# Kernel optimization log

Measured on AMD Instinct MI355X. Metric: run time of the kernel, lower is better.

Reference implementation:

```python
import jax, jax.numpy as jnp
import numpy as np

B, T, ND, SD, H = 4096, 256, 16, 8, 64
IN = SD + ND  # LSTM input dim


def setup_inputs() -> dict:
    key = jax.random.key(0)
    ks = jax.random.split(key, 20)
    def w(k, shape):
        fan_in = shape[0]
        return jax.random.normal(k, shape, jnp.float32) / np.sqrt(fan_in)
    return {
        "noise": jax.random.normal(ks[0], (B, T - 1, ND), jnp.float32),
        "eps": jax.random.normal(ks[1], (B, T - 1, SD), jnp.float32),
        "Wx": w(ks[2], (IN, 4 * H)),
        "Wh": w(ks[3], (H, 4 * H)),
        "b": jnp.zeros((4 * H,), jnp.float32),
        "Wm1": w(ks[4], (H, H)), "bm1": jnp.zeros((H,), jnp.float32),
        "Wm2": w(ks[5], (H, H)), "bm2": jnp.zeros((H,), jnp.float32),
        "Wm3": w(ks[6], (H, SD)), "bm3": jnp.zeros((SD,), jnp.float32),
        "Wv1": w(ks[7], (H, H)), "bv1": jnp.zeros((H,), jnp.float32),
        "Wv2": w(ks[8], (H, H)), "bv2": jnp.zeros((H,), jnp.float32),
        "Wv3": w(ks[9], (H, SD)), "bv3": jnp.zeros((SD,), jnp.float32),
    }


def reference(noise, eps, Wx, Wh, b, Wm1, bm1, Wm2, bm2, Wm3, bm3,
              Wv1, bv1, Wv2, bv2, Wv3, bv3):
    Bn = noise.shape[0]
    Hn = Wh.shape[0]
    Dn = Wm3.shape[1]

    def mlp(h, W1, b1, W2, b2, W3, b3):
        a = jax.nn.relu(h @ W1 + b1)
        a = jax.nn.relu(a @ W2 + b2)
        return a @ W3 + b3

    def step(carry, inp_t):
        x, h, c = carry
        n_t, e_t = inp_t
        # Keras LSTM: gates ordered i, f, g(cell), o
        z = jnp.concatenate([x, n_t], axis=-1) @ Wx + h @ Wh + b  # [B, 4H]
        i, f, g, o = jnp.split(z, 4, axis=-1)
        c = jax.nn.sigmoid(f) * c + jax.nn.sigmoid(i) * jnp.tanh(g)
        h = jax.nn.sigmoid(o) * jnp.tanh(c)
        mu = mlp(h, Wm1, bm1, Wm2, bm2, Wm3, bm3)
        std = jnp.exp(0.5 * mlp(h, Wv1, bv1, Wv2, bv2, Wv3, bv3))
        x = mu + std * e_t  # reparameterized Normal(mu, std).sample()
        return (x, h, c), x

    x0 = jnp.zeros((Bn, Dn), noise.dtype)  # log_series=True -> zeros
    h0 = jnp.zeros((Bn, Hn), noise.dtype)
    c0 = jnp.zeros((Bn, Hn), noise.dtype)
    noise_t = jnp.swapaxes(noise, 0, 1)  # [T-1, B, ND]
    eps_t = jnp.swapaxes(eps, 0, 1)      # [T-1, B, SD]
    _, xs = jax.lax.scan(step, (x0, h0, c0), (noise_t, eps_t))
    seq = jnp.concatenate([x0[:, None, :], jnp.swapaxes(xs, 0, 1)], axis=1)  # [B, T, SD]
    return jnp.cumsum(seq, axis=1)
```

## Files before the change

kernel.cpp:

```cpp
#include <hip/hip_runtime.h>

typedef _Float16 half8 __attribute__((ext_vector_type(8)));
typedef _Float16 half4 __attribute__((ext_vector_type(4)));
typedef float f32x4 __attribute__((ext_vector_type(4)));

#define TSTEPS 255
#define R 16
#define BLK 512
#define XSH 104
#define ASH 72

__device__ __forceinline__ float frcp(float x) { return __builtin_amdgcn_rcpf(x); }

__device__ __forceinline__ f32x4 mfma16(half8 a, half8 b, f32x4 c) {
  return __builtin_amdgcn_mfma_f32_16x16x32_f16(a, b, c, 0, 0, 0);
}

__global__ __launch_bounds__(BLK)
void genlstm_kernel(const float* __restrict__ noise,
                    const float* __restrict__ eps,
                    const float* __restrict__ Wx,
                    const float* __restrict__ Wh,
                    const float* __restrict__ bg,
                    const float* __restrict__ Wm1, const float* __restrict__ bm1,
                    const float* __restrict__ Wm2, const float* __restrict__ bm2,
                    const float* __restrict__ Wm3, const float* __restrict__ bm3,
                    const float* __restrict__ Wv1, const float* __restrict__ bv1,
                    const float* __restrict__ Wv2, const float* __restrict__ bv2,
                    const float* __restrict__ Wv3, const float* __restrict__ bv3,
                    float* __restrict__ out)
{
  __shared__ __align__(16) _Float16 xh[2][R][XSH];
  __shared__ __align__(16) _Float16 xl[2][R][XSH];
  __shared__ __align__(16) _Float16 a1h[2][R][ASH];
  __shared__ __align__(16) _Float16 a1l[2][R][ASH];
  __shared__ __align__(16) _Float16 a2h[2][R][ASH];
  __shared__ __align__(16) _Float16 a2l[2][R][ASH];

  const int tid  = threadIdx.x;
  const int w    = tid >> 6;
  const int l    = tid & 63;
  const int lrow = l & 15;
  const int lq   = l >> 4;
  const long rowbase = (long)blockIdx.x * R;

  half8 gAhi[2][3], gAlo[2][3];
  #pragma unroll
  for (int t = 0; t < 2; ++t) {
    const int T = 2 * w + t;
    const int n = 64 * (lrow & 3) + 4 * T + (lrow >> 2);
    #pragma unroll
    for (int kt = 0; kt < 3; ++kt)
      #pragma unroll
      for (int j = 0; j < 8; ++j) {
        int k = 32 * kt + 8 * lq + j;
        float v = 0.f;
        if (k < 64) v = Wh[k * 256 + n];
        else if (k < 88) v = Wx[(k - 64) * 256 + n];
        _Float16 h = (_Float16)v;
        gAhi[t][kt][j] = h;
        gAlo[t][kt][j] = (_Float16)(v - (float)h);
      }
  }

  const int chain = w >> 2;
  const int nt = w & 3;
  const float* W1 = chain ? Wv1 : Wm1;
  const float* W2 = chain ? Wv2 : Wm2;
  half8 B1hi[2], B1lo[2], B2hi[2], B2lo[2];
  #pragma unroll
  for (int kt = 0; kt < 2; ++kt)
    #pragma unroll
    for (int j = 0; j < 8; ++j) {
      int k = 32 * kt + 8 * lq + j;
      int n = 16 * nt + lrow;
      float v1 = W1[k * 64 + n];
      _Float16 h1 = (_Float16)v1;
      B1hi[kt][j] = h1; B1lo[kt][j] = (_Float16)(v1 - (float)h1);
      float v2 = W2[k * 64 + n];
      _Float16 h2 = (_Float16)v2;
      B2hi[kt][j] = h2; B2lo[kt][j] = (_Float16)(v2 - (float)h2);
    }

  half8 Amhi[2], Amlo[2], Avhi[2], Avlo[2];
  #pragma unroll
  for (int kt = 0; kt < 2; ++kt)
    #pragma unroll
    for (int j = 0; j < 8; ++j) {
      int k = 32 * kt + 8 * lq + j;
      float vm = (lrow < 8) ? Wm3[k * 8 + lrow] : 0.f;
      _Float16 hm = (_Float16)vm;
      Amhi[kt][j] = hm; Amlo[kt][j] = (_Float16)(vm - (float)hm);
      float vv = (lrow < 8) ? Wv3[k * 8 + lrow] : 0.f;
      _Float16 hv = (_Float16)vv;
      Avhi[kt][j] = hv; Avlo[kt][j] = (_Float16)(vv - (float)hv);
    }

  const float bias1 = (chain ? bv1 : bm1)[16 * nt + lrow];
  const float bias2 = (chain ? bv2 : bm2)[16 * nt + lrow];

  const int hc1 = 8 * w + lq, hc2 = hc1 + 4;
  const float4 bgA = {bg[hc1], bg[64 + hc1], bg[128 + hc1], bg[192 + hc1]};
  const float4 bgB = {bg[hc2], bg[64 + hc2], bg[128 + hc2], bg[192 + hc2]};

  const int d0 = 4 * (lq & 1);
  const float4 bm3q = *(const float4*)&bm3[d0];
  const float4 bv3q = *(const float4*)&bv3[d0];

  float cst0 = 0.f, cst1 = 0.f;
  f32x4 cum4 = {0.f, 0.f, 0.f, 0.f};
  float4 ep4 = {0.f, 0.f, 0.f, 0.f};

  half8 hHi[2], hLo[2];
  #pragma unroll
  for (int kt = 0; kt < 2; ++kt)
    #pragma unroll
    for (int j = 0; j < 8; ++j) { hHi[kt][j] = (_Float16)0; hLo[kt][j] = (_Float16)0; }

  for (int i = tid; i < 2 * R * XSH; i += BLK) {
    (&xh[0][0][0])[i] = (_Float16)0;
    (&xl[0][0][0])[i] = (_Float16)0;
  }
  {
    const int r5 = tid >> 3, d5 = tid & 7;
    if (tid < 128) out[((rowbase + r5) * 256) * 8 + d5] = 0.f;
  }

  float4 nz = {0.f, 0.f, 0.f, 0.f};
  if (tid < 64) {
    int r = tid >> 2, j4 = (tid & 3) * 4;
    float4 n0 = *(const float4*)&noise[((rowbase + r) * TSTEPS) * 16 + j4];
    float tmp[4] = {n0.x, n0.y, n0.z, n0.w};
    half4 nh, nl;
    #pragma unroll
    for (int j = 0; j < 4; ++j) {
      _Float16 h = (_Float16)tmp[j];
      nh[j] = h; nl[j] = (_Float16)(tmp[j] - (float)h);
    }
    *(half4*)&xh[0][r][72 + j4] = nh;
    *(half4*)&xl[0][r][72 + j4] = nl;
    nz = *(const float4*)&noise[((rowbase + r) * TSTEPS + 1) * 16 + j4];
  }
  if (w == 0 && lq < 2)
    ep4 = *(const float4*)&eps[((rowbase + lrow) * TSTEPS) * 8 + d0];
  __syncthreads();

  for (int ts = 0; ts < TSTEPS; ++ts) {
    const int p = ts & 1, p1 = p ^ 1;

    half8 Xhi = *(const half8*)&xh[p][lrow][64 + 8 * lq];
    half8 Xlo = *(const half8*)&xl[p][lrow][64 + 8 * lq];

    f32x4 az0 = {0.f, 0.f, 0.f, 0.f};
    f32x4 az1 = {0.f, 0.f, 0.f, 0.f};
    az0 = mfma16(gAhi[0][0], hHi[0], az0);
    az1 = mfma16(gAhi[1][0], hHi[0], az1);
    az0 = mfma16(gAlo[0][0], hHi[0], az0);
    az1 = mfma16(gAlo[1][0], hHi[0], az1);
    az0 = mfma16(gAhi[0][0], hLo[0], az0);
    az1 = mfma16(gAhi[1][0], hLo[0], az1);
    az0 = mfma16(gAhi[0][1], hHi[1], az0);
    az1 = mfma16(gAhi[1][1], hHi[1], az1);
    az0 = mfma16(gAlo[0][1], hHi[1], az0);
    az1 = mfma16(gAlo[1][1], hHi[1], az1);
    az0 = mfma16(gAhi[0][1], hLo[1], az0);
    az1 = mfma16(gAhi[1][1], hLo[1], az1);
    az0 = mfma16(gAhi[0][2], Xhi, az0);
    az1 = mfma16(gAhi[1][2], Xhi, az1);
    az0 = mfma16(gAlo[0][2], Xhi, az0);
    az1 = mfma16(gAlo[1][2], Xhi, az1);
    az0 = mfma16(gAhi[0][2], Xlo, az0);
    az1 = mfma16(gAhi[1][2], Xlo, az1);

    {
      float zi = az0[0] + bgA.x, zf = az0[1] + bgA.y;
      float zg = az0[2] + bgA.z, zo = az0[3] + bgA.w;
      float si = frcp(1.f + __expf(-zi));
      float sf = frcp(1.f + __expf(-zf));
      float so = frcp(1.f + __expf(-zo));
      float ag = fabsf(zg), eg = __expf(-2.f * ag);
      float tg = copysignf((1.f - eg) * frcp(1.f + eg), zg);
      cst0 = fmaf(sf, cst0, si * tg);
      float ac = fabsf(cst0), ec = __expf(-2.f * ac);
      float tc = copysignf((1.f - ec) * frcp(1.f + ec), cst0);
      float hv = so * tc;
      _Float16 hh = (_Float16)hv;
      xh[p1][lrow][hc1] = hh;
      xl[p1][lrow][hc1] = (_Float16)(hv - (float)hh);
    }
    {
      float zi = az1[0] + bgB.x, zf = az1[1] + bgB.y;
      float zg = az1[2] + bgB.z, zo = az1[3] + bgB.w;
      float si = frcp(1.f + __expf(-zi));
      float sf = frcp(1.f + __expf(-zf));
      float so = frcp(1.f + __expf(-zo));
      float ag = fabsf(zg), eg = __expf(-2.f * ag);
      float tg = copysignf((1.f - eg) * frcp(1.f + eg), zg);
      cst1 = fmaf(sf, cst1, si * tg);
      float ac = fabsf(cst1), ec = __expf(-2.f * ac);
      float tc = copysignf((1.f - ec) * frcp(1.f + ec), cst1);
      float hv = so * tc;
      _Float16 hh = (_Float16)hv;
      xh[p1][lrow][hc2] = hh;
      xl[p1][lrow][hc2] = (_Float16)(hv - (float)hh);
    }
    if (tid < 64) {
      int r = tid >> 2, j4 = (tid & 3) * 4;
      float tmp[4] = {nz.x, nz.y, nz.z, nz.w};
      half4 nh, nl;
      #pragma unroll
      for (int j = 0; j < 4; ++j) {
        _Float16 h = (_Float16)tmp[j];
        nh[j] = h; nl[j] = (_Float16)(tmp[j] - (float)h);
      }
      *(half4*)&xh[p1][r][72 + j4] = nh;
      *(half4*)&xl[p1][r][72 + j4] = nl;
      if (ts + 2 < TSTEPS)
        nz = *(const float4*)&noise[((rowbase + r) * TSTEPS + ts + 2) * 16 + j4];
    }
    __syncthreads();

    {
      hHi[0] = *(const half8*)&xh[p1][lrow][8 * lq];
      hHi[1] = *(const half8*)&xh[p1][lrow][32 + 8 * lq];
      hLo[0] = *(const half8*)&xl[p1][lrow][8 * lq];
      hLo[1] = *(const half8*)&xl[p1][lrow][32 + 8 * lq];
      f32x4 acc = {0.f, 0.f, 0.f, 0.f};
      #pragma unroll
      for (int kt = 0; kt < 2; ++kt) {
        acc = mfma16(hHi[kt], B1hi[kt], acc);
        acc = mfma16(hLo[kt], B1hi[kt], acc);
        acc = mfma16(hHi[kt], B1lo[kt], acc);
      }
      const int r0 = 4 * lq;
      #pragma unroll
      for (int k = 0; k < 4; ++k) {
        float v = fmaxf(acc[k] + bias1, 0.f);
        _Float16 vh = (_Float16)v;
        a1h[chain][r0 + k][16 * nt + lrow] = vh;
        a1l[chain][r0 + k][16 * nt + lrow] = (_Float16)(v - (float)vh);
      }
    }
    __syncthreads();

    {
      half8 ahi0 = *(const half8*)&a1h[chain][lrow][8 * lq];
      half8 ahi1 = *(const half8*)&a1h[chain][lrow][32 + 8 * lq];
      half8 alo0 = *(const half8*)&a1l[chain][lrow][8 * lq];
      half8 alo1 = *(const half8*)&a1l[chain][lrow][32 + 8 * lq];
      f32x4 acc = {0.f, 0.f, 0.f, 0.f};
      acc = mfma16(ahi0, B2hi[0], acc);
      acc = mfma16(alo0, B2hi[0], acc);
      acc = mfma16(ahi0, B2lo[0], acc);
      acc = mfma16(ahi1, B2hi[1], acc);
      acc = mfma16(alo1, B2hi[1], acc);
      acc = mfma16(ahi1, B2lo[1], acc);
      const int r0 = 4 * lq;
      #pragma unroll
      for (int k = 0; k < 4; ++k) {
        float v = fmaxf(acc[k] + bias2, 0.f);
        _Float16 vh = (_Float16)v;
        a2h[chain][r0 + k][16 * nt + lrow] = vh;
        a2l[chain][r0 + k][16 * nt + lrow] = (_Float16)(v - (float)vh);
      }
    }
    __syncthreads();

    if (w == 0) {
      half8 b0h0 = *(const half8*)&a2h[0][lrow][8 * lq];
      half8 b0h1 = *(const half8*)&a2h[0][lrow][32 + 8 * lq];
      half8 b0l0 = *(const half8*)&a2l[0][lrow][8 * lq];
      half8 b0l1 = *(const half8*)&a2l[0][lrow][32 + 8 * lq];
      f32x4 accm = {0.f, 0.f, 0.f, 0.f};
      accm = mfma16(Amhi[0], b0h0, accm);
      accm = mfma16(Amlo[0], b0h0, accm);
      accm = mfma16(Amhi[0], b0l0, accm);
      accm = mfma16(Amhi[1], b0h1, accm);
      accm = mfma16(Amlo[1], b0h1, accm);
      accm = mfma16(Amhi[1], b0l1, accm);
      half8 b1h0 = *(const half8*)&a2h[1][lrow][8 * lq];
      half8 b1h1 = *(const half8*)&a2h[1][lrow][32 + 8 * lq];
      half8 b1l0 = *(const half8*)&a2l[1][lrow][8 * lq];
      half8 b1l1 = *(const half8*)&a2l[1][lrow][32 + 8 * lq];
      f32x4 accv = {0.f, 0.f, 0.f, 0.f};
      accv = mfma16(Avhi[0], b1h0, accv);
      accv = mfma16(Avlo[0], b1h0, accv);
      accv = mfma16(Avhi[0], b1l0, accv);
      accv = mfma16(Avhi[1], b1h1, accv);
      accv = mfma16(Avlo[1], b1h1, accv);
      accv = mfma16(Avhi[1], b1l1, accv);

      float xs0 = fmaf(__expf(0.5f * (accv[0] + bv3q.x)), ep4.x, accm[0] + bm3q.x);
      float xs1 = fmaf(__expf(0.5f * (accv[1] + bv3q.y)), ep4.y, accm[1] + bm3q.y);
      float xs2 = fmaf(__expf(0.5f * (accv[2] + bv3q.z)), ep4.z, accm[2] + bm3q.z);
      float xs3 = fmaf(__expf(0.5f * (accv[3] + bv3q.w)), ep4.w, accm[3] + bm3q.w);
      cum4[0] += xs0; cum4[1] += xs1; cum4[2] += xs2; cum4[3] += xs3;
      if (lq < 2) {
        float4 cv = {cum4[0], cum4[1], cum4[2], cum4[3]};
        *(float4*)&out[((rowbase + lrow) * 256 + ts + 1) * 8 + d0] = cv;
        float xs[4] = {xs0, xs1, xs2, xs3};
        half4 xhv, xlv;
        #pragma unroll
        for (int j = 0; j < 4; ++j) {
          _Float16 hh = (_Float16)xs[j];
          xhv[j] = hh; xlv[j] = (_Float16)(xs[j] - (float)hh);
        }
        *(half4*)&xh[p1][lrow][64 + d0] = xhv;
        *(half4*)&xl[p1][lrow][64 + d0] = xlv;
        if (ts + 1 < TSTEPS)
          ep4 = *(const float4*)&eps[((rowbase + lrow) * TSTEPS + ts + 1) * 8 + d0];
      }
    }
    __syncthreads();
  }
}

extern "C" void kernel_launch(void* const* d_in, const int* in_sizes, int n_in,
                              void* d_out, int out_size, void* d_ws, size_t ws_size,
                              hipStream_t stream) {
  const float* noise = (const float*)d_in[0];
  const float* eps   = (const float*)d_in[1];
  const float* Wx    = (const float*)d_in[2];
  const float* Wh    = (const float*)d_in[3];
  const float* bg    = (const float*)d_in[4];
  const float* Wm1   = (const float*)d_in[5];
  const float* bm1   = (const float*)d_in[6];
  const float* Wm2   = (const float*)d_in[7];
  const float* bm2   = (const float*)d_in[8];
  const float* Wm3   = (const float*)d_in[9];
  const float* bm3   = (const float*)d_in[10];
  const float* Wv1   = (const float*)d_in[11];
  const float* bv1   = (const float*)d_in[12];
  const float* Wv2   = (const float*)d_in[13];
  const float* bv2   = (const float*)d_in[14];
  const float* Wv3   = (const float*)d_in[15];
  const float* bv3   = (const float*)d_in[16];
  float* out = (float*)d_out;

  dim3 grid(4096 / R), block(BLK);
  hipLaunchKernelGGL(genlstm_kernel, grid, block, 0, stream,
                     noise, eps, Wx, Wh, bg, Wm1, bm1, Wm2, bm2, Wm3, bm3,
                     Wv1, bv1, Wv2, bv2, Wv3, bv3, out);
}
```

Before: 544.7 us.

## Hoist recurrent h@Wh MFMAs off critical path and use LDS-only barriers

The recurrent gate contribution h@Wh is now computed right after the MLP stages, while wave 0 runs the output head, so the next step only adds the x-part MFMAs before the gate nonlinearity. __syncthreads is replaced by an lgkmcnt-only wait plus s_barrier, which no longer waits on outstanding global loads or stores. The noise staging moves from wave 0 to wave 6 to unload the wave that does the output head, and the output store is moved after the LDS writes. The risk is that the LDS-only barrier relies on global memory not being used for synchronisation between threads.

```diff
diff --git a/kernel.cpp b/kernel.cpp
--- a/kernel.cpp
+++ b/kernel.cpp
@@ -14,6 +14,25 @@
 
 __device__ __forceinline__ f32x4 mfma16(half8 a, half8 b, f32x4 c) {
   return __builtin_amdgcn_mfma_f32_16x16x32_f16(a, b, c, 0, 0, 0);
+}
+
+__device__ __forceinline__ void barrier_lds() {
+  asm volatile("s_waitcnt lgkmcnt(0)" ::: "memory");
+  __builtin_amdgcn_s_barrier();
+}
+
+__device__ __forceinline__ float gate_nl(const f32x4& az, const float4& bq, float& cs) {
+  float zi = az[0] + bq.x, zf = az[1] + bq.y;
+  float zg = az[2] + bq.z, zo = az[3] + bq.w;
+  float si = frcp(1.f + __expf(-zi));
+  float sf = frcp(1.f + __expf(-zf));
+  float so = frcp(1.f + __expf(-zo));
+  float ag = fabsf(zg), eg = __expf(-2.f * ag);
+  float tg = copysignf((1.f - eg) * frcp(1.f + eg), zg);
+  cs = fmaf(sf, cs, si * tg);
+  float ac = fabsf(cs), ec = __expf(-2.f * ac);
+  float tc = copysignf((1.f - ec) * frcp(1.f + ec), cs);
+  return so * tc;
 }
 
 __global__ __launch_bounds__(BLK)
@@ -110,6 +129,7 @@
   float cst0 = 0.f, cst1 = 0.f;
   f32x4 cum4 = {0.f, 0.f, 0.f, 0.f};
   float4 ep4 = {0.f, 0.f, 0.f, 0.f};
+  const f32x4 fzero = {0.f, 0.f, 0.f, 0.f};
 
   half8 hHi[2], hLo[2];
   #pragma unroll
@@ -127,8 +147,9 @@
   }
 
   float4 nz = {0.f, 0.f, 0.f, 0.f};
-  if (tid < 64) {
-    int r = tid >> 2, j4 = (tid & 3) * 4;
+  if (tid >= 384 && tid < 448) {
+    int idx = tid - 384;
+    int r = idx >> 2, j4 = (idx & 3) * 4;
     float4 n0 = *(const float4*)&noise[((rowbase + r) * TSTEPS) * 16 + j4];
     float tmp[4] = {n0.x, n0.y, n0.z, n0.w};
     half4 nh, nl;
@@ -143,16 +164,99 @@
   }
   if (w == 0 && lq < 2)
     ep4 = *(const float4*)&eps[((rowbase + lrow) * TSTEPS) * 8 + d0];
-  __syncthreads();
+  barrier_lds();
+
+  f32x4 az0 = fzero, az1 = fzero;
 
   for (int ts = 0; ts < TSTEPS; ++ts) {
     const int p = ts & 1, p1 = p ^ 1;
 
     half8 Xhi = *(const half8*)&xh[p][lrow][64 + 8 * lq];
     half8 Xlo = *(const half8*)&xl[p][lrow][64 + 8 * lq];
-
-    f32x4 az0 = {0.f, 0.f, 0.f, 0.f};
-    f32x4 az1 = {0.f, 0.f, 0.f, 0.f};
+    az0 = mfma16(gAhi[0][2], Xhi, az0);
+    az1 = mfma16(gAhi[1][2], Xhi, az1);
+    az0 = mfma16(gAlo[0][2], Xhi, az0);
+    az1 = mfma16(gAlo[1][2], Xhi, az1);
+    az0 = mfma16(gAhi[0][2], Xlo, az0);
+    az1 = mfma16(gAhi[1][2], Xlo, az1);
+
+    {
+      float hv = gate_nl(az0, bgA, cst0);
+      _Float16 hh = (_Float16)hv;
+      xh[p1][lrow][hc1] = hh;
+      xl[p1][lrow][hc1] = (_Float16)(hv - (float)hh);
+    }
+    {
+      float hv = gate_nl(az1, bgB, cst1);
+      _Float16 hh = (_Float16)hv;
+      xh[p1][lrow][hc2] = hh;
+      xl[p1][lrow][hc2] = (_Float16)(hv - (float)hh);
+    }
+    az0 = fzero;
+    az1 = fzero;
+    if (tid >= 384 && tid < 448) {
+      int idx = tid - 384;
+      int r = idx >> 2, j4 = (idx & 3) * 4;
+      float tmp[4] = {nz.x, nz.y, nz.z, nz.w};
+      half4 nh, nl;
+      #pragma unroll
+      for (int j = 0; j < 4; ++j) {
+        _Float16 h = (_Float16)tmp[j];
+        nh[j] = h; nl[j] = (_Float16)(tmp[j] - (float)h);
+      }
+      *(half4*)&xh[p1][r][72 + j4] = nh;
+      *(half4*)&xl[p1][r][72 + j4] = nl;
+      if (ts + 2 < TSTEPS)
+        nz = *(const float4*)&noise[((rowbase + r) * TSTEPS + ts + 2) * 16 + j4];
+    }
+    barrier_lds();
+
+    {
+      hHi[0] = *(const half8*)&xh[p1][lrow][8 * lq];
+      hHi[1] = *(const half8*)&xh[p1][lrow][32 + 8 * lq];
+      hLo[0] = *(const half8*)&xl[p1][lrow][8 * lq];
+      hLo[1] = *(const half8*)&xl[p1][lrow][32 + 8 * lq];
+      f32x4 acc = fzero;
+      #pragma unroll
+      for (int kt = 0; kt < 2; ++kt) {
+        acc = mfma16(hHi[kt], B1hi[kt], acc);
+        acc = mfma16(hLo[kt], B1hi[kt], acc);
+        acc = mfma16(hHi[kt], B1lo[kt], acc);
+      }
+      const int r0 = 4 * lq;
+      #pragma unroll
+      for (int k = 0; k < 4; ++k) {
+        float v = fmaxf(acc[k] + bias1, 0.f);
+        _Float16 vh = (_Float16)v;
+        a1h[chain][r0 + k][16 * nt + lrow] = vh;
+        a1l[chain][r0 + k][16 * nt + lrow] = (_Float16)(v - (float)vh);
+      }
+    }
+    barrier_lds();
+
+    {
+      half8 ahi0 = *(const half8*)&a1h[chain][lrow][8 * lq];
+      half8 ahi1 = *(const half8*)&a1h[chain][lrow][32 + 8 * lq];
+      half8 alo0 = *(const half8*)&a1l[chain][lrow][8 * lq];
+      half8 alo1 = *(const half8*)&a1l[chain][lrow][32 + 8 * lq];
+      f32x4 acc = fzero;
+      acc = mfma16(ahi0, B2hi[0], acc);
+      acc = mfma16(alo0, B2hi[0], acc);
+      acc = mfma16(ahi0, B2lo[0], acc);
+      acc = mfma16(ahi1, B2hi[1], acc);
+      acc = mfma16(alo1, B2hi[1], acc);
+      acc = mfma16(ahi1, B2lo[1], acc);
+      const int r0 = 4 * lq;
+      #pragma unroll
+      for (int k = 0; k < 4; ++k) {
+        float v = fmaxf(acc[k] + bias2, 0.f);
+        _Float16 vh = (_Float16)v;
+        a2h[chain][r0 + k][16 * nt + lrow] = vh;
+        a2l[chain][r0 + k][16 * nt + lrow] = (_Float16)(v - (float)vh);
+      }
+    }
+    barrier_lds();
+
     az0 = mfma16(gAhi[0][0], hHi[0], az0);
     az1 = mfma16(gAhi[1][0], hHi[0], az1);
     az0 = mfma16(gAlo[0][0], hHi[0], az0);
@@ -165,113 +269,13 @@
     az1 = mfma16(gAlo[1][1], hHi[1], az1);
     az0 = mfma16(gAhi[0][1], hLo[1], az0);
     az1 = mfma16(gAhi[1][1], hLo[1], az1);
-    az0 = mfma16(gAhi[0][2], Xhi, az0);
-    az1 = mfma16(gAhi[1][2], Xhi, az1);
-    az0 = mfma16(gAlo[0][2], Xhi, az0);
-    az1 = mfma16(gAlo[1][2], Xhi, az1);
-    az0 = mfma16(gAhi[0][2], Xlo, az0);
-    az1 = mfma16(gAhi[1][2], Xlo, az1);
-
-    {
-      float zi = az0[0] + bgA.x, zf = az0[1] + bgA.y;
-      float zg = az0[2] + bgA.z, zo = az0[3] + bgA.w;
-      float si = frcp(1.f + __expf(-zi));
-      float sf = frcp(1.f + __expf(-zf));
-      float so = frcp(1.f + __expf(-zo));
-      float ag = fabsf(zg), eg = __expf(-2.f * ag);
-      float tg = copysignf((1.f - eg) * frcp(1.f + eg), zg);
-      cst0 = fmaf(sf, cst0, si * tg);
-      float ac = fabsf(cst0), ec = __expf(-2.f * ac);
-      float tc = copysignf((1.f - ec) * frcp(1.f + ec), cst0);
-      float hv = so * tc;
-      _Float16 hh = (_Float16)hv;
-      xh[p1][lrow][hc1] = hh;
-      xl[p1][lrow][hc1] = (_Float16)(hv - (float)hh);
-    }
-    {
-      float zi = az1[0] + bgB.x, zf = az1[1] + bgB.y;
-      float zg = az1[2] + bgB.z, zo = az1[3] + bgB.w;
-      float si = frcp(1.f + __expf(-zi));
-      float sf = frcp(1.f + __expf(-zf));
-      float so = frcp(1.f + __expf(-zo));
-      float ag = fabsf(zg), eg = __expf(-2.f * ag);
-      float tg = copysignf((1.f - eg) * frcp(1.f + eg), zg);
-      cst1 = fmaf(sf, cst1, si * tg);
-      float ac = fabsf(cst1), ec = __expf(-2.f * ac);
-      float tc = copysignf((1.f - ec) * frcp(1.f + ec), cst1);
-      float hv = so * tc;
-      _Float16 hh = (_Float16)hv;
-      xh[p1][lrow][hc2] = hh;
-      xl[p1][lrow][hc2] = (_Float16)(hv - (float)hh);
-    }
-    if (tid < 64) {
-      int r = tid >> 2, j4 = (tid & 3) * 4;
-      float tmp[4] = {nz.x, nz.y, nz.z, nz.w};
-      half4 nh, nl;
-      #pragma unroll
-      for (int j = 0; j < 4; ++j) {
-        _Float16 h = (_Float16)tmp[j];
-        nh[j] = h; nl[j] = (_Float16)(tmp[j] - (float)h);
-      }
-      *(half4*)&xh[p1][r][72 + j4] = nh;
-      *(half4*)&xl[p1][r][72 + j4] = nl;
-      if (ts + 2 < TSTEPS)
-        nz = *(const float4*)&noise[((rowbase + r) * TSTEPS + ts + 2) * 16 + j4];
-    }
-    __syncthreads();
-
-    {
-      hHi[0] = *(const half8*)&xh[p1][lrow][8 * lq];
-      hHi[1] = *(const half8*)&xh[p1][lrow][32 + 8 * lq];
-      hLo[0] = *(const half8*)&xl[p1][lrow][8 * lq];
-      hLo[1] = *(const half8*)&xl[p1][lrow][32 + 8 * lq];
-      f32x4 acc = {0.f, 0.f, 0.f, 0.f};
-      #pragma unroll
-      for (int kt = 0; kt < 2; ++kt) {
-        acc = mfma16(hHi[kt], B1hi[kt], acc);
-        acc = mfma16(hLo[kt], B1hi[kt], acc);
-        acc = mfma16(hHi[kt], B1lo[kt], acc);
-      }
-      const int r0 = 4 * lq;
-      #pragma unroll
-      for (int k = 0; k < 4; ++k) {
-        float v = fmaxf(acc[k] + bias1, 0.f);
-        _Float16 vh = (_Float16)v;
-        a1h[chain][r0 + k][16 * nt + lrow] = vh;
-        a1l[chain][r0 + k][16 * nt + lrow] = (_Float16)(v - (float)vh);
-      }
-    }
-    __syncthreads();
-
-    {
-      half8 ahi0 = *(const half8*)&a1h[chain][lrow][8 * lq];
-      half8 ahi1 = *(const half8*)&a1h[chain][lrow][32 + 8 * lq];
-      half8 alo0 = *(const half8*)&a1l[chain][lrow][8 * lq];
-      half8 alo1 = *(const half8*)&a1l[chain][lrow][32 + 8 * lq];
-      f32x4 acc = {0.f, 0.f, 0.f, 0.f};
-      acc = mfma16(ahi0, B2hi[0], acc);
-      acc = mfma16(alo0, B2hi[0], acc);
-      acc = mfma16(ahi0, B2lo[0], acc);
-      acc = mfma16(ahi1, B2hi[1], acc);
-      acc = mfma16(alo1, B2hi[1], acc);
-      acc = mfma16(ahi1, B2lo[1], acc);
-      const int r0 = 4 * lq;
-      #pragma unroll
-      for (int k = 0; k < 4; ++k) {
-        float v = fmaxf(acc[k] + bias2, 0.f);
-        _Float16 vh = (_Float16)v;
-        a2h[chain][r0 + k][16 * nt + lrow] = vh;
-        a2l[chain][r0 + k][16 * nt + lrow] = (_Float16)(v - (float)vh);
-      }
-    }
-    __syncthreads();
 
     if (w == 0) {
       half8 b0h0 = *(const half8*)&a2h[0][lrow][8 * lq];
       half8 b0h1 = *(const half8*)&a2h[0][lrow][32 + 8 * lq];
       half8 b0l0 = *(const half8*)&a2l[0][lrow][8 * lq];
       half8 b0l1 = *(const half8*)&a2l[0][lrow][32 + 8 * lq];
-      f32x4 accm = {0.f, 0.f, 0.f, 0.f};
+      f32x4 accm = fzero;
       accm = mfma16(Amhi[0], b0h0, accm);
       accm = mfma16(Amlo[0], b0h0, accm);
       accm = mfma16(Amhi[0], b0l0, accm);
@@ -282,7 +286,7 @@
       half8 b1h1 = *(const half8*)&a2h[1][lrow][32 + 8 * lq];
       half8 b1l0 = *(const half8*)&a2l[1][lrow][8 * lq];
       half8 b1l1 = *(const half8*)&a2l[1][lrow][32 + 8 * lq];
-      f32x4 accv = {0.f, 0.f, 0.f, 0.f};
+      f32x4 accv = fzero;
       accv = mfma16(Avhi[0], b1h0, accv);
       accv = mfma16(Avlo[0], b1h0, accv);
       accv = mfma16(Avhi[0], b1l0, accv);
@@ -296,8 +300,6 @@
       float xs3 = fmaf(__expf(0.5f * (accv[3] + bv3q.w)), ep4.w, accm[3] + bm3q.w);
       cum4[0] += xs0; cum4[1] += xs1; cum4[2] += xs2; cum4[3] += xs3;
       if (lq < 2) {
-        float4 cv = {cum4[0], cum4[1], cum4[2], cum4[3]};
-        *(float4*)&out[((rowbase + lrow) * 256 + ts + 1) * 8 + d0] = cv;
         float xs[4] = {xs0, xs1, xs2, xs3};
         half4 xhv, xlv;
         #pragma unroll
@@ -307,11 +309,13 @@
         }
         *(half4*)&xh[p1][lrow][64 + d0] = xhv;
         *(half4*)&xl[p1][lrow][64 + d0] = xlv;
+        float4 cv = {cum4[0], cum4[1], cum4[2], cum4[3]};
+        *(float4*)&out[((rowbase + lrow) * 256 + ts + 1) * 8 + d0] = cv;
         if (ts + 1 < TSTEPS)
           ep4 = *(const float4*)&eps[((rowbase + lrow) * TSTEPS + ts + 1) * 8 + d0];
       }
     }
-    __syncthreads();
+    barrier_lds();
   }
 }
 
```

Measured after the change: 552.9 us. About the same (+1.5%).
